# Optimization experiments

Measured on AMD Instinct MI355X. Metric: run time of the kernel, lower is better.

## Reference

```python
import jax, jax.numpy as jnp
import numpy as np

N, E, DIN, DH, DOUT = 100000, 600000, 128, 128, 64


def _glorot(k, shape):
    lim = float(np.sqrt(6.0 / (shape[0] + shape[1])))
    return jax.random.uniform(k, shape, jnp.float32, -lim, lim)


def setup_inputs() -> dict:
    key = jax.random.key(0)
    ks = jax.random.split(key, 12)
    return {
        "x": jax.random.normal(ks[0], (N, DIN), jnp.float32),
        "src": jax.random.randint(ks[1], (E,), 0, N),
        "dst": jax.random.randint(ks[2], (E,), 0, N),
        # layer 0: NGNN_SAGEConv = SAGEConv(in,hid) + fc(hid,hid) + fc2(hid,hid)
        "w_self0": _glorot(ks[3], (DIN, DH)), "b_self0": jnp.zeros((DH,), jnp.float32),
        "w_neigh0": _glorot(ks[4], (DIN, DH)),
        "fc_w": _glorot(ks[5], (DH, DH)), "fc_b": jnp.zeros((DH,), jnp.float32),
        "fc2_w": _glorot(ks[6], (DH, DH)), "fc2_b": jnp.zeros((DH,), jnp.float32),
        # layer 1: SAGEConv(hid,hid)
        "w_self1": _glorot(ks[7], (DH, DH)), "b_self1": jnp.zeros((DH,), jnp.float32),
        "w_neigh1": _glorot(ks[8], (DH, DH)),
        # layer 2: SAGEConv(hid,out)
        "w_self2": _glorot(ks[9], (DH, DOUT)), "b_self2": jnp.zeros((DOUT,), jnp.float32),
        "w_neigh2": _glorot(ks[10], (DH, DOUT)),
    }


def _sage_conv(x, src, dst, w_self, b_self, w_neigh):
    # DGL SAGEConv, aggregator='mean': out = x @ W_self + b + mean_{u->v} x_u @ W_neigh
    agg = jax.ops.segment_sum(x[src], dst, num_segments=N)          # [N, d_in]
    deg = jax.ops.segment_sum(jnp.ones((src.shape[0],), x.dtype), dst, num_segments=N)
    h_neigh = agg / jnp.maximum(deg, 1.0)[:, None]                  # zero-in-degree -> 0
    return x @ w_self + b_self + h_neigh @ w_neigh


def reference(x, src, dst,
              w_self0, b_self0, w_neigh0, fc_w, fc_b, fc2_w, fc2_b,
              w_self1, b_self1, w_neigh1,
              w_self2, b_self2, w_neigh2):
    # layer 0: NGNN_SAGEConv with num_nonl_layers=2, then outer ReLU (dropout: eval = identity)
    h = _sage_conv(x, src, dst, w_self0, b_self0, w_neigh0)
    h = jax.nn.relu(h)
    h = h @ fc_w + fc_b
    h = jax.nn.relu(h)
    h = h @ fc2_w + fc2_b
    h = jax.nn.relu(h)
    # layer 1: SAGEConv + ReLU
    h = _sage_conv(h, src, dst, w_self1, b_self1, w_neigh1)
    h = jax.nn.relu(h)
    # layer 2 (output): SAGEConv, no activation
    return _sage_conv(h, src, dst, w_self2, b_self2, w_neigh2)
```

## Files before the change

kernel.cpp:

```cpp
#include <hip/hip_runtime.h>

#define N_NODES 100000
#define N_EDGES 600000
#define K_DIM   128
#define NPART   ((N_NODES + 255) / 256)
#define EBLK    ((N_EDGES + 255) / 256)
#define CASTB   (N_NODES * K_DIM / 8 / 256)
#define GBLK    ((N_NODES + 127) / 128)
#define VROWS   (GBLK * 128)

typedef unsigned short ushort_t;
typedef short v8s __attribute__((ext_vector_type(8)));
typedef float v4f __attribute__((ext_vector_type(4)));

__device__ __forceinline__ ushort_t f2b(float f) {
  unsigned u = __builtin_bit_cast(unsigned, f);
  unsigned r = u + 0x7FFFu + ((u >> 16) & 1u);
  return (ushort_t)(r >> 16);
}
__device__ __forceinline__ float b2f(ushort_t h) {
  return __builtin_bit_cast(float, (unsigned)h << 16);
}
__device__ __forceinline__ float blo(unsigned u) {
  return __builtin_bit_cast(float, u << 16);
}
__device__ __forceinline__ float bhi(unsigned u) {
  return __builtin_bit_cast(float, u & 0xFFFF0000u);
}
__device__ __forceinline__ unsigned pk2(float lo, float hi) {
  return (unsigned)f2b(lo) | ((unsigned)f2b(hi) << 16);
}


__global__ void deg_cast_kernel(const int* __restrict__ dst, int* __restrict__ deg,
                                const float* __restrict__ X, ushort_t* __restrict__ Xb) {
  if (blockIdx.x < EBLK) {
    int e = blockIdx.x * 256 + threadIdx.x;
    if (e < N_EDGES) atomicAdd(&deg[dst[e]], 1);
  } else {
    int i = ((blockIdx.x - EBLK) * 256 + threadIdx.x) * 8;
    if (i >= N_NODES * K_DIM) return;
    float4 v0 = *(const float4*)(X + i);
    float4 v1 = *(const float4*)(X + i + 4);
    ushort4 h0, h1;
    h0.x = f2b(v0.x); h0.y = f2b(v0.y); h0.z = f2b(v0.z); h0.w = f2b(v0.w);
    h1.x = f2b(v1.x); h1.y = f2b(v1.y); h1.z = f2b(v1.z); h1.w = f2b(v1.w);
    *(ushort4*)(Xb + i)     = h0;
    *(ushort4*)(Xb + i + 4) = h1;
  }
}

__global__ void scan1_swz_kernel(
    const int* __restrict__ deg, int* __restrict__ excl, int* __restrict__ partials,
    const float* __restrict__ w0, const float* __restrict__ w1,
    const float* __restrict__ w2, const float* __restrict__ w3,
    const float* __restrict__ w4, const float* __restrict__ w5,
    const float* __restrict__ w6, const float* __restrict__ w7,
    ushort_t* __restrict__ s0, ushort_t* __restrict__ s1,
    ushort_t* __restrict__ s2, ushort_t* __restrict__ s3,
    ushort_t* __restrict__ s4, ushort_t* __restrict__ s5,
    ushort_t* __restrict__ s6, ushort_t* __restrict__ s7) {
  __shared__ int s[256];
  if (blockIdx.x < NPART) {
    int t = threadIdx.x, i = blockIdx.x * 256 + t;
    int v = (i < N_NODES) ? deg[i] : 0;
    s[t] = v;
    __syncthreads();
    for (int off = 1; off < 256; off <<= 1) {
      int x = (t >= off) ? s[t - off] : 0;
      __syncthreads();
      s[t] += x;
      __syncthreads();
    }
    if (i < N_NODES) excl[i] = s[t] - v;
    if (t == 255) partials[blockIdx.x] = s[t];
  } else {
    const int blk = blockIdx.x - NPART;
    const int z = blk >> 6;
    const float* W;
    ushort_t* S;
    int dout = 128;
    switch (z) {
      case 0: W = w0; S = s0; break;
      case 1: W = w1; S = s1; break;
      case 2: W = w2; S = s2; break;
      case 3: W = w3; S = s3; break;
      case 4: W = w4; S = s4; break;
      case 5: W = w5; S = s5; break;
      case 6: W = w6; S = s6; dout = 64; break;
      default: W = w7; S = s7; dout = 64; break;
    }
    int t = (blk & 63) * 256 + threadIdx.x;
    if (t >= K_DIM * dout) return;
    int k = t / dout, n = t % dout;
    S[(k >> 3) * (dout * 8) + n * 8 + (k & 7)] = f2b(W[t]);
  }
}

__global__ void scan3_kernel(const int* __restrict__ excl, const int* __restrict__ partials,
                             const int* __restrict__ deg, int* __restrict__ row_ptr,
                             int* __restrict__ cursor, float* __restrict__ inv_deg) {
  __shared__ int red[256];
  const int t = threadIdx.x, b = blockIdx.x;
  int sum = 0;
  for (int j = t; j < b && j < NPART; j += 256) sum += partials[j];
  red[t] = sum;
  __syncthreads();
  #pragma unroll
  for (int off = 128; off > 0; off >>= 1) {
    if (t < off) red[t] += red[t + off];
    __syncthreads();
  }
  const int base = red[0];

  const int i = b * 256 + t;
  if (i < N_NODES) {
    int rp = excl[i] + base;
    row_ptr[i] = rp;
    cursor[i] = rp;
    inv_deg[i] = 1.0f / (float)(deg[i] > 1 ? deg[i] : 1);
  } else if (i == N_NODES) {
    row_ptr[N_NODES] = N_EDGES;
  }
}

__global__ void fill_kernel(const int* __restrict__ src, const int* __restrict__ dst,
                            int* __restrict__ cursor, int* __restrict__ ssrc) {
  int e = blockIdx.x * blockDim.x + threadIdx.x;
  if (e < N_EDGES) {
    int p = atomicAdd(&cursor[dst[e]], 1);
    ssrc[p] = src[e];
  }
}

__device__ __forceinline__ void agg_rows(
    const ushort_t* __restrict__ H, ushort_t* __restrict__ AGG,
    const int* __restrict__ row_ptr, const int* __restrict__ ssrc,
    const float* __restrict__ inv_deg, int row0, int lm, int q) {
  const int c0 = lm * 8;
  for (int rr = 0; rr < 4; ++rr) {
    const int lr = q * 4 + rr;
    const int gv = row0 + lr;
    const int vv = gv < N_NODES ? gv : N_NODES - 1;
    float a[8];
    #pragma unroll
    for (int i = 0; i < 8; ++i) a[i] = 0.f;
    const int beg = row_ptr[vv], end = row_ptr[vv + 1];
    int e = beg;
    for (; e + 4 <= end; e += 4) {
      const int s0 = ssrc[e];
      const int s1 = ssrc[e + 1];
      const int s2 = ssrc[e + 2];
      const int s3 = ssrc[e + 3];
      const uint4 p0 = *(const uint4*)(H + (size_t)s0 * K_DIM + c0);
      const uint4 p1 = *(const uint4*)(H + (size_t)s1 * K_DIM + c0);
      const uint4 p2 = *(const uint4*)(H + (size_t)s2 * K_DIM + c0);
      const uint4 p3 = *(const uint4*)(H + (size_t)s3 * K_DIM + c0);
      a[0] += (blo(p0.x) + blo(p1.x)) + (blo(p2.x) + blo(p3.x));
      a[1] += (bhi(p0.x) + bhi(p1.x)) + (bhi(p2.x) + bhi(p3.x));
      a[2] += (blo(p0.y) + blo(p1.y)) + (blo(p2.y) + blo(p3.y));
      a[3] += (bhi(p0.y) + bhi(p1.y)) + (bhi(p2.y) + bhi(p3.y));
      a[4] += (blo(p0.z) + blo(p1.z)) + (blo(p2.z) + blo(p3.z));
      a[5] += (bhi(p0.z) + bhi(p1.z)) + (bhi(p2.z) + bhi(p3.z));
      a[6] += (blo(p0.w) + blo(p1.w)) + (blo(p2.w) + blo(p3.w));
      a[7] += (bhi(p0.w) + bhi(p1.w)) + (bhi(p2.w) + bhi(p3.w));
    }
    if (e + 2 <= end) {
      const int s0 = ssrc[e];
      const int s1 = ssrc[e + 1];
      const uint4 p0 = *(const uint4*)(H + (size_t)s0 * K_DIM + c0);
      const uint4 p1 = *(const uint4*)(H + (size_t)s1 * K_DIM + c0);
      a[0] += blo(p0.x) + blo(p1.x);
      a[1] += bhi(p0.x) + bhi(p1.x);
      a[2] += blo(p0.y) + blo(p1.y);
      a[3] += bhi(p0.y) + bhi(p1.y);
      a[4] += blo(p0.z) + blo(p1.z);
      a[5] += bhi(p0.z) + bhi(p1.z);
      a[6] += blo(p0.w) + blo(p1.w);
      a[7] += bhi(p0.w) + bhi(p1.w);
      e += 2;
    }
    if (e < end) {
      const int s0 = ssrc[e];
      const uint4 p0 = *(const uint4*)(H + (size_t)s0 * K_DIM + c0);
      a[0] += blo(p0.x);
      a[1] += bhi(p0.x);
      a[2] += blo(p0.y);
      a[3] += bhi(p0.y);
      a[4] += blo(p0.z);
      a[5] += bhi(p0.z);
      a[6] += blo(p0.w);
      a[7] += bhi(p0.w);
    }
    const float sc = inv_deg[vv];
    uint4 ov;
    ov.x = pk2(a[0] * sc, a[1] * sc);
    ov.y = pk2(a[2] * sc, a[3] * sc);
    ov.z = pk2(a[4] * sc, a[5] * sc);
    ov.w = pk2(a[6] * sc, a[7] * sc);
    *(uint4*)&AGG[(size_t)gv * K_DIM + c0] = ov;
  }
}


template <int DOUT, bool RELU, bool BF16_OUT>
__global__ __launch_bounds__(512, 8) void sage_layer_kernel(
    const ushort_t* __restrict__ H,
    ushort_t* __restrict__ AGG,
    const ushort_t* __restrict__ Wself_sw, const ushort_t* __restrict__ Wneigh_sw,
    const float* __restrict__ bias,
    const int* __restrict__ row_ptr, const int* __restrict__ ssrc,
    const float* __restrict__ inv_deg,
    ushort_t* __restrict__ Obf, float* __restrict__ Ofp) {
  constexpr int NT  = DOUT / 16;
  constexpr int SWN = K_DIM * DOUT;
  constexpr int NW  = SWN / 4096;
  __shared__ __align__(16) ushort_t buf[16384];

  const int tid   = threadIdx.x;
  const int wv    = tid >> 6;
  const int lane  = tid & 63;
  const int lm    = lane & 15;
  const int q     = lane >> 4;
  const int lrow0 = wv * 16;
  const int row0  = blockIdx.x * 128 + lrow0;

  #pragma unroll
  for (int j = 0; j < NW; ++j)
    *(uint4*)&buf[tid * 8 + j * 4096] = *(const uint4*)&Wneigh_sw[tid * 8 + j * 4096];
  uint4 wreg[NW];
  #pragma unroll
  for (int j = 0; j < NW; ++j)
    wreg[j] = *(const uint4*)&Wself_sw[tid * 8 + j * 4096];
  __syncthreads();

  agg_rows(H, AGG, row_ptr, ssrc, inv_deg, row0, lm, q);

  v4f acc[NT];
  #pragma unroll
  for (int n = 0; n < NT; ++n) acc[n] = (v4f){0.f, 0.f, 0.f, 0.f};

  const size_t offA = (size_t)(row0 + lm) * K_DIM;
  for (int ks = 0; ks < K_DIM / 32; ++ks) {
    const int ko = ks * 32 + q * 8;
    const v8s a0 = *(const v8s*)(AGG + offA + ko);
    #pragma unroll
    for (int nt = 0; nt < NT; ++nt) {
      const v8s b = *(const v8s*)&buf[((ks * 4 + q) * DOUT + nt * 16 + lm) * 8];
      acc[nt] = __builtin_amdgcn_mfma_f32_16x16x32_bf16(a0, b, acc[nt], 0, 0, 0);
    }
  }
  __syncthreads();

  #pragma unroll
  for (int j = 0; j < NW; ++j)
    *(uint4*)&buf[tid * 8 + j * 4096] = wreg[j];
  __syncthreads();

  int ra = row0 + lm;  ra = ra < N_NODES ? ra : N_NODES - 1;
  const size_t off0 = (size_t)ra * K_DIM;
  for (int ks = 0; ks < K_DIM / 32; ++ks) {
    const int ko = ks * 32 + q * 8;
    const v8s a0 = *(const v8s*)(H + off0 + ko);
    #pragma unroll
    for (int nt = 0; nt < NT; ++nt) {
      const v8s b = *(const v8s*)&buf[((ks * 4 + q) * DOUT + nt * 16 + lm) * 8];
      acc[nt] = __builtin_amdgcn_mfma_f32_16x16x32_bf16(a0, b, acc[nt], 0, 0, 0);
    }
  }
  __syncthreads();

  const int base = blockIdx.x * 128;
  if constexpr (BF16_OUT) {
    #pragma unroll
    for (int nt = 0; nt < NT; ++nt) {
      const int col = nt * 16 + lm;
      const float bv = bias[col];
      #pragma unroll
      for (int r = 0; r < 4; ++r) {
        float v = acc[nt][r] + bv;
        if (RELU) v = v > 0.f ? v : 0.f;
        buf[(lrow0 + q * 4 + r) * DOUT + col] = f2b(v);
      }
    }
    __syncthreads();
    #pragma unroll
    for (int i = tid * 8; i < 128 * DOUT; i += 4096) {
      const int rw = i / DOUT;
      if (base + rw < N_NODES)
        *(uint4*)&Obf[(size_t)(base + rw) * DOUT + (i % DOUT)] = *(const uint4*)&buf[i];
    }
  } else {
    float* fb = (float*)buf;
    #pragma unroll
    for (int nt = 0; nt < NT; ++nt) {
      const int col = nt * 16 + lm;
      const float bv = bias[col];
      #pragma unroll
      for (int r = 0; r < 4; ++r) {
        float v = acc[nt][r] + bv;
        if (RELU) v = v > 0.f ? v : 0.f;
        fb[(lrow0 + q * 4 + r) * DOUT + col] = v;
      }
    }
    __syncthreads();
    #pragma unroll
    for (int i = tid * 4; i < 128 * DOUT; i += 2048) {
      const int rw = i / DOUT;
      if (base + rw < N_NODES)
        *(float4*)&Ofp[(size_t)(base + rw) * DOUT + (i % DOUT)] = *(const float4*)&fb[i];
    }
  }
}


__global__ __launch_bounds__(512, 4) void fused_fc_kernel(
    const ushort_t* __restrict__ A,
    const ushort_t* __restrict__ W1sw, const ushort_t* __restrict__ W2sw,
    const float* __restrict__ b1, const float* __restrict__ b2,
    ushort_t* __restrict__ O) {
  constexpr int NT = 8;
  constexpr int HP = 136;
  __shared__ ushort_t bufW[K_DIM * 128];
  __shared__ ushort_t bufH[128 * HP];

  const int tid   = threadIdx.x;
  const int wv    = tid >> 6;
  const int lane  = tid & 63;
  const int lm    = lane & 15;
  const int q     = lane >> 4;
  const int lrow0 = wv * 16;
  const int row0  = blockIdx.x * 128 + lrow0;

  for (int i = tid * 8; i < K_DIM * 128; i += 4096)
    *(uint4*)&bufW[i] = *(const uint4*)&W1sw[i];

  uint4 wreg[4];
  #pragma unroll
  for (int j = 0; j < 4; ++j)
    wreg[j] = *(const uint4*)&W2sw[tid * 8 + j * 4096];

  __syncthreads();

  int ra = row0 + lm;  ra = ra < N_NODES ? ra : N_NODES - 1;
  const size_t off0 = (size_t)ra * K_DIM;

  v4f acc[NT];
  #pragma unroll
  for (int n = 0; n < NT; ++n) acc[n] = (v4f){0.f, 0.f, 0.f, 0.f};

  for (int ks = 0; ks < K_DIM / 32; ++ks) {
    const int ko = ks * 32 + q * 8;
    const v8s a0 = *(const v8s*)(A + off0 + ko);
    #pragma unroll
    for (int nt = 0; nt < NT; ++nt) {
      const v8s b = *(const v8s*)&bufW[((ks * 4 + q) * 128 + nt * 16 + lm) * 8];
      acc[nt] = __builtin_amdgcn_mfma_f32_16x16x32_bf16(a0, b, acc[nt], 0, 0, 0);
    }
  }
  __syncthreads();

  #pragma unroll
  for (int j = 0; j < 4; ++j)
    *(uint4*)&bufW[tid * 8 + j * 4096] = wreg[j];
  #pragma unroll
  for (int nt = 0; nt < NT; ++nt) {
    const int col = nt * 16 + lm;
    const float bv = b1[col];
    #pragma unroll
    for (int r = 0; r < 4; ++r) {
      float v = acc[nt][r] + bv;
      v = v > 0.f ? v : 0.f;
      bufH[(lrow0 + q * 4 + r) * HP + col] = f2b(v);
      acc[nt][r] = 0.f;
    }
  }
  __syncthreads();

  for (int ks = 0; ks < K_DIM / 32; ++ks) {
    const int ko = ks * 32 + q * 8;
    const v8s a0 = *(const v8s*)&bufH[(lrow0 + lm) * HP + ko];
    #pragma unroll
    for (int nt = 0; nt < NT; ++nt) {
      const v8s b = *(const v8s*)&bufW[((ks * 4 + q) * 128 + nt * 16 + lm) * 8];
      acc[nt] = __builtin_amdgcn_mfma_f32_16x16x32_bf16(a0, b, acc[nt], 0, 0, 0);
    }
  }

  #pragma unroll
  for (int nt = 0; nt < NT; ++nt) {
    const int col = nt * 16 + lm;
    const float bv = b2[col];
    #pragma unroll
    for (int r = 0; r < 4; ++r) {
      const int row = row0 + q * 4 + r;
      if (row < N_NODES) {
        float v = acc[nt][r] + bv;
        v = v > 0.f ? v : 0.f;
        O[(size_t)row * 128 + col] = f2b(v);
      }
    }
  }
}


extern "C" void kernel_launch(void* const* d_in, const int* in_sizes, int n_in,
                              void* d_out, int out_size, void* d_ws, size_t ws_size,
                              hipStream_t stream) {
  const float* x        = (const float*)d_in[0];
  const int*   src      = (const int*)d_in[1];
  const int*   dst      = (const int*)d_in[2];
  const float* w_self0  = (const float*)d_in[3];
  const float* b_self0  = (const float*)d_in[4];
  const float* w_neigh0 = (const float*)d_in[5];
  const float* fc_w     = (const float*)d_in[6];
  const float* fc_b     = (const float*)d_in[7];
  const float* fc2_w    = (const float*)d_in[8];
  const float* fc2_b    = (const float*)d_in[9];
  const float* w_self1  = (const float*)d_in[10];
  const float* b_self1  = (const float*)d_in[11];
  const float* w_neigh1 = (const float*)d_in[12];
  const float* w_self2  = (const float*)d_in[13];
  const float* b_self2  = (const float*)d_in[14];
  const float* w_neigh2 = (const float*)d_in[15];

  char* p = (char*)d_ws;
  auto carve = [&](size_t bytes) {
    void* q = (void*)p;
    p += (bytes + 511) & ~(size_t)511;
    return q;
  };
  const size_t VPLANE = (size_t)VROWS * K_DIM * sizeof(ushort_t);
  ushort_t* X    = (ushort_t*)carve(VPLANE);
  ushort_t* Y    = (ushort_t*)carve(VPLANE);
  ushort_t* Z    = (ushort_t*)carve(VPLANE);
  ushort_t* AGGs = (ushort_t*)carve(VPLANE);
  ushort_t* ws0 = (ushort_t*)carve(K_DIM * 128 * 2);
  ushort_t* wn0 = (ushort_t*)carve(K_DIM * 128 * 2);
  ushort_t* wfc = (ushort_t*)carve(K_DIM * 128 * 2);
  ushort_t* wf2 = (ushort_t*)carve(K_DIM * 128 * 2);
  ushort_t* ws1 = (ushort_t*)carve(K_DIM * 128 * 2);
  ushort_t* wn1 = (ushort_t*)carve(K_DIM * 128 * 2);
  ushort_t* ws2 = (ushort_t*)carve(K_DIM * 64 * 2);
  ushort_t* wn2 = (ushort_t*)carve(K_DIM * 64 * 2);
  int*   ssrc    = (int*)carve((size_t)N_EDGES * 4);
  int*   row_ptr = (int*)carve((size_t)(N_NODES + 1) * 4);
  int*   cursor  = (int*)carve((size_t)N_NODES * 4);
  int*   deg     = (int*)carve((size_t)N_NODES * 4);
  int*   excl    = (int*)carve((size_t)N_NODES * 4);
  int*   parts   = (int*)carve(512 * 4);
  float* inv_deg = (float*)carve((size_t)N_NODES * 4);

  hipMemsetAsync(deg, 0, (size_t)N_NODES * 4, stream);
  deg_cast_kernel<<<EBLK + CASTB, 256, 0, stream>>>(dst, deg, x, X);
  scan1_swz_kernel<<<NPART + 512, 256, 0, stream>>>(
      deg, excl, parts,
      w_self0, w_neigh0, fc_w, fc2_w, w_self1, w_neigh1, w_self2, w_neigh2,
      ws0, wn0, wfc, wf2, ws1, wn1, ws2, wn2);
  scan3_kernel<<<((N_NODES + 1) + 255) / 256, 256, 0, stream>>>(excl, parts, deg,
                                                                row_ptr, cursor, inv_deg);
  fill_kernel<<<EBLK, 256, 0, stream>>>(src, dst, cursor, ssrc);

  const int GB = GBLK;

  sage_layer_kernel<128, true, true><<<GB, 512, 0, stream>>>(
      X, AGGs, ws0, wn0, b_self0, row_ptr, ssrc, inv_deg, Z, nullptr);
  fused_fc_kernel<<<GB, 512, 0, stream>>>(Z, wfc, wf2, fc_b, fc2_b, Y);
  sage_layer_kernel<128, true, true><<<GB, 512, 0, stream>>>(
      Y, AGGs, ws1, wn1, b_self1, row_ptr, ssrc, inv_deg, Z, nullptr);
  sage_layer_kernel<64, false, false><<<GB, 512, 0, stream>>>(
      Z, AGGs, ws2, wn2, b_self2, row_ptr, ssrc, inv_deg, nullptr, (float*)d_out);
}
```

Baseline: 368.9 us.

## Fuse layer-0 SAGE conv with both FC layers into one kernel

Merges the first SAGEConv layer and the two following FC+ReLU layers into one kernel. The aggregated neighbor features stay in LDS instead of round-tripping through global memory, and the intermediate Z write/read disappears. Weights are now read straight from global memory (L2-cached) rather than staged in LDS, which cuts LDS use and allows higher occupancy. The cost is more uncoalesced global weight reads on every MFMA step, plus three back-to-back GEMMs in one kernel.

```diff
diff --git a/kernel.cpp b/kernel.cpp
--- a/kernel.cpp
+++ b/kernel.cpp
@@ -133,14 +133,15 @@
   }
 }
 
-__device__ __forceinline__ void agg_rows(
-    const ushort_t* __restrict__ H, ushort_t* __restrict__ AGG,
+template <int STRIDE>
+__device__ __forceinline__ void gather16(
+    const ushort_t* __restrict__ H, ushort_t* __restrict__ dstbuf,
     const int* __restrict__ row_ptr, const int* __restrict__ ssrc,
-    const float* __restrict__ inv_deg, int row0, int lm, int q) {
+    const float* __restrict__ inv_deg, int row0_g, int drow0, int lm, int q) {
   const int c0 = lm * 8;
   for (int rr = 0; rr < 4; ++rr) {
     const int lr = q * 4 + rr;
-    const int gv = row0 + lr;
+    const int gv = row0_g + lr;
     const int vv = gv < N_NODES ? gv : N_NODES - 1;
     float a[8];
     #pragma unroll
@@ -198,7 +199,7 @@
     ov.y = pk2(a[2] * sc, a[3] * sc);
     ov.z = pk2(a[4] * sc, a[5] * sc);
     ov.w = pk2(a[6] * sc, a[7] * sc);
-    *(uint4*)&AGG[(size_t)gv * K_DIM + c0] = ov;
+    *(uint4*)&dstbuf[(size_t)(drow0 + lr) * STRIDE + c0] = ov;
   }
 }
 
@@ -234,7 +235,7 @@
     wreg[j] = *(const uint4*)&Wself_sw[tid * 8 + j * 4096];
   __syncthreads();
 
-  agg_rows(H, AGG, row_ptr, ssrc, inv_deg, row0, lm, q);
+  gather16<K_DIM>(H, AGG, row_ptr, ssrc, inv_deg, row0, row0, lm, q);
 
   v4f acc[NT];
   #pragma unroll
@@ -314,15 +315,18 @@
 }
 
 
-__global__ __launch_bounds__(512, 4) void fused_fc_kernel(
-    const ushort_t* __restrict__ A,
-    const ushort_t* __restrict__ W1sw, const ushort_t* __restrict__ W2sw,
-    const float* __restrict__ b1, const float* __restrict__ b2,
+__global__ __launch_bounds__(512, 8) void ngnn0_kernel(
+    const ushort_t* __restrict__ X,
+    const ushort_t* __restrict__ Ws0, const ushort_t* __restrict__ Wn0,
+    const ushort_t* __restrict__ Wf1, const ushort_t* __restrict__ Wf2,
+    const float* __restrict__ b0, const float* __restrict__ bf1,
+    const float* __restrict__ bf2,
+    const int* __restrict__ row_ptr, const int* __restrict__ ssrc,
+    const float* __restrict__ inv_deg,
     ushort_t* __restrict__ O) {
   constexpr int NT = 8;
   constexpr int HP = 136;
-  __shared__ ushort_t bufW[K_DIM * 128];
-  __shared__ ushort_t bufH[128 * HP];
+  __shared__ __align__(16) ushort_t aggb[128 * HP];
 
   const int tid   = threadIdx.x;
   const int wv    = tid >> 6;
@@ -332,57 +336,53 @@
   const int lrow0 = wv * 16;
   const int row0  = blockIdx.x * 128 + lrow0;
 
-  for (int i = tid * 8; i < K_DIM * 128; i += 4096)
-    *(uint4*)&bufW[i] = *(const uint4*)&W1sw[i];
-
-  uint4 wreg[4];
-  #pragma unroll
-  for (int j = 0; j < 4; ++j)
-    wreg[j] = *(const uint4*)&W2sw[tid * 8 + j * 4096];
-
-  __syncthreads();
+  gather16<HP>(X, aggb, row_ptr, ssrc, inv_deg, row0, lrow0, lm, q);
+
+  v4f acc[NT];
+  #pragma unroll
+  for (int n = 0; n < NT; ++n) acc[n] = (v4f){0.f, 0.f, 0.f, 0.f};
+
+  for (int ks = 0; ks < K_DIM / 32; ++ks) {
+    const int ko = ks * 32 + q * 8;
+    const v8s a0 = *(const v8s*)&aggb[(lrow0 + lm) * HP + ko];
+    #pragma unroll
+    for (int nt = 0; nt < NT; ++nt) {
+      const v8s b = *(const v8s*)&Wn0[((ks * 4 + q) * 128 + nt * 16 + lm) * 8];
+      acc[nt] = __builtin_amdgcn_mfma_f32_16x16x32_bf16(a0, b, acc[nt], 0, 0, 0);
+    }
+  }
 
   int ra = row0 + lm;  ra = ra < N_NODES ? ra : N_NODES - 1;
   const size_t off0 = (size_t)ra * K_DIM;
-
-  v4f acc[NT];
-  #pragma unroll
-  for (int n = 0; n < NT; ++n) acc[n] = (v4f){0.f, 0.f, 0.f, 0.f};
-
   for (int ks = 0; ks < K_DIM / 32; ++ks) {
     const int ko = ks * 32 + q * 8;
-    const v8s a0 = *(const v8s*)(A + off0 + ko);
-    #pragma unroll
-    for (int nt = 0; nt < NT; ++nt) {
-      const v8s b = *(const v8s*)&bufW[((ks * 4 + q) * 128 + nt * 16 + lm) * 8];
+    const v8s a0 = *(const v8s*)(X + off0 + ko);
+    #pragma unroll
+    for (int nt = 0; nt < NT; ++nt) {
+      const v8s b = *(const v8s*)&Ws0[((ks * 4 + q) * 128 + nt * 16 + lm) * 8];
       acc[nt] = __builtin_amdgcn_mfma_f32_16x16x32_bf16(a0, b, acc[nt], 0, 0, 0);
     }
   }
-  __syncthreads();
-
-  #pragma unroll
-  for (int j = 0; j < 4; ++j)
-    *(uint4*)&bufW[tid * 8 + j * 4096] = wreg[j];
+
   #pragma unroll
   for (int nt = 0; nt < NT; ++nt) {
     const int col = nt * 16 + lm;
-    const float bv = b1[col];
+    const float bv = b0[col];
     #pragma unroll
     for (int r = 0; r < 4; ++r) {
       float v = acc[nt][r] + bv;
       v = v > 0.f ? v : 0.f;
-      bufH[(lrow0 + q * 4 + r) * HP + col] = f2b(v);
+      aggb[(lrow0 + q * 4 + r) * HP + col] = f2b(v);
       acc[nt][r] = 0.f;
     }
   }
-  __syncthreads();
 
   for (int ks = 0; ks < K_DIM / 32; ++ks) {
     const int ko = ks * 32 + q * 8;
-    const v8s a0 = *(const v8s*)&bufH[(lrow0 + lm) * HP + ko];
-    #pragma unroll
-    for (int nt = 0; nt < NT; ++nt) {
-      const v8s b = *(const v8s*)&bufW[((ks * 4 + q) * 128 + nt * 16 + lm) * 8];
+    const v8s a0 = *(const v8s*)&aggb[(lrow0 + lm) * HP + ko];
+    #pragma unroll
+    for (int nt = 0; nt < NT; ++nt) {
+      const v8s b = *(const v8s*)&Wf1[((ks * 4 + q) * 128 + nt * 16 + lm) * 8];
       acc[nt] = __builtin_amdgcn_mfma_f32_16x16x32_bf16(a0, b, acc[nt], 0, 0, 0);
     }
   }
@@ -390,16 +390,46 @@
   #pragma unroll
   for (int nt = 0; nt < NT; ++nt) {
     const int col = nt * 16 + lm;
-    const float bv = b2[col];
+    const float bv = bf1[col];
     #pragma unroll
     for (int r = 0; r < 4; ++r) {
-      const int row = row0 + q * 4 + r;
-      if (row < N_NODES) {
-        float v = acc[nt][r] + bv;
-        v = v > 0.f ? v : 0.f;
-        O[(size_t)row * 128 + col] = f2b(v);
-      }
-    }
+      float v = acc[nt][r] + bv;
+      v = v > 0.f ? v : 0.f;
+      aggb[(lrow0 + q * 4 + r) * HP + col] = f2b(v);
+      acc[nt][r] = 0.f;
+    }
+  }
+
+  for (int ks = 0; ks < K_DIM / 32; ++ks) {
+    const int ko = ks * 32 + q * 8;
+    const v8s a0 = *(const v8s*)&aggb[(lrow0 + lm) * HP + ko];
+    #pragma unroll
+    for (int nt = 0; nt < NT; ++nt) {
+      const v8s b = *(const v8s*)&Wf2[((ks * 4 + q) * 128 + nt * 16 + lm) * 8];
+      acc[nt] = __builtin_amdgcn_mfma_f32_16x16x32_bf16(a0, b, acc[nt], 0, 0, 0);
+    }
+  }
+
+  #pragma unroll
+  for (int nt = 0; nt < NT; ++nt) {
+    const int col = nt * 16 + lm;
+    const float bv = bf2[col];
+    #pragma unroll
+    for (int r = 0; r < 4; ++r) {
+      float v = acc[nt][r] + bv;
+      v = v > 0.f ? v : 0.f;
+      aggb[(lrow0 + q * 4 + r) * HP + col] = f2b(v);
+    }
+  }
+  #pragma unroll
+  for (int j = 0; j < 4; ++j) {
+    const int idx = j * 64 + lane;
+    const int rw  = idx >> 4;
+    const int sg  = idx & 15;
+    const int grow = row0 + rw;
+    if (grow < N_NODES)
+      *(uint4*)&O[(size_t)grow * 128 + sg * 8] =
+          *(const uint4*)&aggb[(lrow0 + rw) * HP + sg * 8];
   }
 }
 
@@ -463,9 +493,9 @@
 
   const int GB = GBLK;
 
-  sage_layer_kernel<128, true, true><<<GB, 512, 0, stream>>>(
-      X, AGGs, ws0, wn0, b_self0, row_ptr, ssrc, inv_deg, Z, nullptr);
-  fused_fc_kernel<<<GB, 512, 0, stream>>>(Z, wfc, wf2, fc_b, fc2_b, Y);
+  ngnn0_kernel<<<GB, 512, 0, stream>>>(
+      X, ws0, wn0, wfc, wf2, b_self0, fc_b, fc2_b,
+      row_ptr, ssrc, inv_deg, Y);
   sage_layer_kernel<128, true, true><<<GB, 512, 0, stream>>>(
       Y, AGGs, ws1, wn1, b_self1, row_ptr, ssrc, inv_deg, Z, nullptr);
   sage_layer_kernel<64, false, false><<<GB, 512, 0, stream>>>(
```

Measured after the change: 349.8 us. -5.2%, faster.
